# Kernel optimization log

Hardware: AMD Instinct MI355X
Metric: run time of the kernel (lower is better)

The kernel has to match this reference:

```python
import jax, jax.numpy as jnp
import numpy as np

B, L, DIN, DOUT, H, N, NLAYERS, NRES, NSPECIES = 32, 2048, 5, 5, 256, 32, 4, 3, 100


def conv1d(x, w, b, pad):
    # x: (B, Cin, L), w: (Cout, Cin, K)
    y = jax.lax.conv_general_dilated(x, w, (1,), [(pad, pad)], dimension_numbers=('NCH', 'OIH', 'NCH'))
    return y + b[None, :, None]


def layer_norm_c(x, g, b):
    # LayerNorm over channel dim of (B, H, L) (matches norm(x.transpose(-1,-2)).transpose(-1,-2))
    mu = x.mean(1, keepdims=True)
    v = ((x - mu) ** 2).mean(1, keepdims=True)
    return (x - mu) / jnp.sqrt(v + 1e-5) * g[None, :, None] + b[None, :, None]


def dss_layer(x, log_dt, lam_re, lam_im, W_re, W_im, D, glu_w, glu_b):
    # Bidirectional diagonal state-space (DSS) layer, transposed layout (B, H, L).
    Bb, Hh, Ll = x.shape
    dt = jnp.exp(log_dt)                                  # (H,)
    lam = lam_re + 1j * lam_im                            # (N,) with Re(lam) < 0
    pos = jnp.arange(Ll)
    # Vandermonde: E[h,n,l] = exp(dt[h] * lam[n] * l)
    E = jnp.exp(dt[:, None, None] * lam[None, :, None] * pos[None, None, :])  # (H,N,L) complex
    W = W_re + 1j * W_im                                  # (2,H,N) fwd/bwd kernels
    k = jnp.einsum('chn,hnl->chl', W, E).real             # (2,H,L)
    zpad = jnp.zeros_like(k[0])
    k2 = jnp.concatenate([k[0], zpad], -1) + jnp.concatenate([zpad, k[1][:, ::-1]], -1)  # (H,2L)
    # FFT circular conv of length 2L -> linear conv, keep first L
    y = jnp.fft.irfft(jnp.fft.rfft(x, 2 * Ll) * jnp.fft.rfft(k2, 2 * Ll)[None], 2 * Ll)[..., :Ll]
    y = y + D[None, :, None] * x
    y = jax.nn.gelu(y, approximate=False)
    # postact GLU via position-wise linear H -> 2H
    z = jnp.einsum('oh,bhl->bol', glu_w, y) + glu_b[None, :, None]
    return z[:, :Hh] * jax.nn.sigmoid(z[:, Hh:])


def setup_inputs():
    key = jax.random.key(0)
    ks = jax.random.split(key, 20)
    g = lambda i, shape, s=0.05: jax.random.normal(ks[i], shape, jnp.float32) * s
    inp = {}
    inp['x'] = jax.random.normal(ks[0], (B, DIN, L), jnp.float32)
    inp['xs'] = jax.random.randint(ks[1], (B,), 0, NSPECIES)
    inp['enc_w'] = g(2, (H, DIN, 15))
    inp['enc_b'] = jnp.zeros((H,), jnp.float32)
    inp['res_w1'] = g(3, (NRES, H, H, 3), 0.02)
    inp['res_b1'] = jnp.zeros((NRES, H), jnp.float32)
    inp['res_w2'] = g(4, (NRES, H, H, 3), 0.02)
    inp['res_b2'] = jnp.zeros((NRES, H), jnp.float32)
    inp['log_dt'] = jax.random.uniform(ks[5], (NLAYERS, H), jnp.float32, float(np.log(1e-3)), float(np.log(1e-1)))
    inp['lam_re'] = -(0.1 + jax.random.uniform(ks[6], (NLAYERS, N), jnp.float32))
    inp['lam_im'] = jnp.broadcast_to(jnp.pi * jnp.arange(N, dtype=jnp.float32), (NLAYERS, N)) + 0.0
    inp['W_re'] = g(7, (NLAYERS, 2, H, N), 0.1)
    inp['W_im'] = g(8, (NLAYERS, 2, H, N), 0.1)
    inp['D'] = g(9, (NLAYERS, H), 1.0)
    inp['glu_w'] = g(10, (NLAYERS, 2 * H, H))
    inp['glu_b'] = jnp.zeros((NLAYERS, 2 * H), jnp.float32)
    inp['ln_g'] = jnp.ones((NLAYERS, H), jnp.float32)
    inp['ln_b'] = jnp.zeros((NLAYERS, H), jnp.float32)
    inp['dec_w'] = g(11, (DOUT, H, 15))
    inp['dec_b'] = jnp.zeros((DOUT,), jnp.float32)
    inp['sp_emb'] = g(12, (NSPECIES, H), 0.02)
    inp['h1_w'] = g(13, (128, 256)); inp['h1_b'] = jnp.zeros((128,), jnp.float32)
    inp['h2_w'] = g(14, (64, 128)); inp['h2_b'] = jnp.zeros((64,), jnp.float32)
    inp['h3_w'] = g(15, (32, 64)); inp['h3_b'] = jnp.zeros((32,), jnp.float32)
    inp['h4_w'] = g(16, (1, 32)); inp['h4_b'] = jnp.zeros((1,), jnp.float32)
    return inp


def _forward(x, xs, enc_w, enc_b, res_w1, res_b1, res_w2, res_b2, log_dt, lam_re, lam_im, W_re, W_im, D, glu_w, glu_b, ln_g, ln_b, dec_w, dec_b, sp_emb, h1_w, h1_b, h2_w, h2_b, h3_w, h3_b, h4_w, h4_b):
    h = conv1d(x, enc_w, enc_b, 7)
    for i in range(NRES):  # L1Block resnet stack (dropout/BN are identity at eval)
        r = jax.nn.relu(conv1d(h, res_w1[i], res_b1[i], 1))
        r = conv1d(r, res_w2[i], res_b2[i], 1)
        h = jax.nn.relu(r + h)
    for i in range(NLAYERS):  # post-norm DSS blocks
        z = dss_layer(h, log_dt[i], lam_re[i], lam_im[i], W_re[i], W_im[i], D[i], glu_w[i], glu_b[i])
        h = layer_norm_c(z + h, ln_g[i], ln_b[i])
    h = h + sp_emb[xs][:, :, None]  # species encoder (embed_before=False)
    seq_emb = h
    agg = h.mean(-1)  # (B, H)
    r = jax.nn.elu(agg @ h1_w.T + h1_b)
    r = jax.nn.elu(r @ h2_w.T + h2_b)
    r = jax.nn.elu(r @ h3_w.T + h3_b)
    reg_y = r @ h4_w.T + h4_b
    dec = conv1d(h, dec_w, dec_b, 7)
    return dec, seq_emb, reg_y


def reference(x, xs, enc_w, enc_b, res_w1, res_b1, res_w2, res_b2, log_dt, lam_re, lam_im, W_re, W_im, D, glu_w, glu_b, ln_g, ln_b, dec_w, dec_b, sp_emb, h1_w, h1_b, h2_w, h2_b, h3_w, h3_b, h4_w, h4_b):
    return _forward(x, xs, enc_w, enc_b, res_w1, res_b1, res_w2, res_b2, log_dt, lam_re, lam_im, W_re, W_im, D, glu_w, glu_b, ln_g, ln_b, dec_w, dec_b, sp_emb, h1_w, h1_b, h2_w, h2_b, h3_w, h3_b, h4_w, h4_b)
```

## Files before the change

kernel.cpp:

```cpp
#include <hip/hip_runtime.h>
#include <math.h>

#define B 32
#define L 2048
#define DIN 5
#define DOUT 5
#define H 256
#define NST 32
#define NLAYERS 4
#define NRES 3
#define CHUNK 128
#define NCH 16
#define LSEQ (B*H*L)

typedef __attribute__((ext_vector_type(8))) _Float16 half8;
typedef __attribute__((ext_vector_type(4))) float f32x4;

__device__ __forceinline__ float gelu_exact(float v) {
    return 0.5f * v * (1.0f + erff(v * 0.7071067811865475f));
}
#define SWZ(r) ((((r) ^ ((r) >> 2)) & 3))
#define LDIDX(l, c) ((l)*281 + ((c)>>5)*35 + ((c)&31))

__global__ void k_wenc(const float* __restrict__ ew, _Float16* __restrict__ wenc) {
    int idx = blockIdx.x*256 + threadIdx.x;
    if (idx >= 256*96) return;
    int o = idx / 96, kk = idx % 96;
    int ci = kk >> 4, k = kk & 15;
    float v = (ci < DIN && k < 15) ? ew[(o*DIN + ci)*15 + k] : 0.f;
    wenc[idx] = (_Float16)v;
}

__global__ __launch_bounds__(256) void k_enc(const float* __restrict__ x,
        const _Float16* __restrict__ wenc, const float* __restrict__ bias,
        _Float16* __restrict__ out) {
    __shared__ _Float16 a_lds[3*128*32];
    __shared__ _Float16 b_lds[3*128*32];
    const int tid = threadIdx.x;
    const int mbase = blockIdx.x * 128;
    const int oh = blockIdx.y;
    const int b = mbase >> 11;
    const int lbase = mbase & 2047;
    const int lane = tid & 63;
    const int w = tid >> 6;
    const int wm = (w >> 1) * 64, wn = (w & 1) * 64;
    const int fr = lane & 15, kg = lane >> 4;

    #pragma unroll
    for (int i = 0; i < 6; ++i) {
        int g = i*256 + tid;
        int r = g / 12, rem = g % 12;
        int ks = rem >> 2, q = rem & 3;
        int kk0 = ks*32 + q*8;
        int ci = kk0 >> 4, k0 = kk0 & 15;
        half8 va;
        #pragma unroll
        for (int e = 0; e < 8; ++e) {
            int k = k0 + e;
            int l = lbase + r - 7 + k;
            float v = (ci < DIN && k < 15 && l >= 0 && l < L)
                        ? x[((size_t)(b*DIN + ci))*L + l] : 0.f;
            va[e] = (_Float16)v;
        }
        *(half8*)&a_lds[ks*4096 + r*32 + ((q ^ SWZ(r))*8)] = va;
        uint4 vb = *(const uint4*)&wenc[(size_t)(oh*128 + r)*96 + kk0];
        *(uint4*)&b_lds[ks*4096 + r*32 + ((q ^ SWZ(r))*8)] = vb;
    }
    __syncthreads();
    f32x4 acc[4][4];
    #pragma unroll
    for (int i = 0; i < 4; ++i)
        #pragma unroll
        for (int j = 0; j < 4; ++j)
            #pragma unroll
            for (int k = 0; k < 4; ++k) acc[i][j][k] = 0.f;
    #pragma unroll
    for (int ks = 0; ks < 3; ++ks) {
        half8 af[4], bfr[4];
        #pragma unroll
        for (int mf = 0; mf < 4; ++mf) {
            int ra = wm + mf*16 + fr;
            af[mf] = *(const half8*)&a_lds[ks*4096 + ra*32 + ((kg ^ SWZ(ra))*8)];
        }
        #pragma unroll
        for (int nf = 0; nf < 4; ++nf) {
            int rb = wn + nf*16 + fr;
            bfr[nf] = *(const half8*)&b_lds[ks*4096 + rb*32 + ((kg ^ SWZ(rb))*8)];
        }
        #pragma unroll
        for (int mf = 0; mf < 4; ++mf)
            #pragma unroll
            for (int nf = 0; nf < 4; ++nf)
                acc[mf][nf] = __builtin_amdgcn_mfma_f32_16x16x32_f16(af[mf], bfr[nf], acc[mf][nf], 0, 0, 0);
    }
    #pragma unroll
    for (int nf = 0; nf < 4; ++nf) {
        int o = oh*128 + wn + nf*16 + fr;
        float bo = bias[o];
        #pragma unroll
        for (int mf = 0; mf < 4; ++mf)
            #pragma unroll
            for (int rg = 0; rg < 4; ++rg) {
                size_t m = (size_t)mbase + wm + mf*16 + kg*4 + rg;
                out[m*256 + o] = (_Float16)(acc[mf][nf][rg] + bo);
            }
// ... 180 lines not shown
__global__ __launch_bounds__(128) void k_wzp(const float4* __restrict__ zw,
        _Float16* __restrict__ zp) {
    int hh = blockIdx.x;
    int t = threadIdx.x;
    int dn = t >> 1, c = t & 1, dir = dn >> 5, n = dn & 31;
    float4 z4 = zw[hh*NST + n];
    float zre = z4.x, zim = z4.y;
    _Float16* dst = &zp[(size_t)hh*16384 + t*128];
    float cr = 1.f, ci = 0.f;
    for (int p = 0; p < 128; ++p) {
        float val = c ? ci : cr;
        dst[dir ? p : (127 - p)] = (_Float16)val;
        float nr = cr*zre - ci*zim;
        float ni = cr*zim + ci*zre;
        cr = nr; ci = ni;
    }
}

__global__ __launch_bounds__(128) void k_wkern(const float* __restrict__ log_dt,
        const float* __restrict__ lam_re, const float* __restrict__ lam_im,
        const float* __restrict__ W_re, const float* __restrict__ W_im,
        _Float16* __restrict__ wbig, int layer) {
    __shared__ float kf[128], kb[128];
    __shared__ float E[128*129];
    const int hh = blockIdx.x;
    const int t = threadIdx.x;
    float dt = expf(log_dt[layer*H + hh]);
    float skf = 0.f, skb = 0.f;
    for (int n = 0; n < 32; ++n) {
        float a  = dt * lam_re[layer*NST + n];
        float bi = dt * lam_im[layer*NST + n];
        float wfr = W_re[((layer*2+0)*H + hh)*NST + n];
        float wfi = W_im[((layer*2+0)*H + hh)*NST + n];
        float wbr = W_re[((layer*2+1)*H + hh)*NST + n];
        float wbi = W_im[((layer*2+1)*H + hh)*NST + n];
        float e0 = expf(a*t), s0, c0; sincosf(bi*t, &s0, &c0);
        float zr0 = e0*c0, zi0 = e0*s0;
        skf = fmaf(wfr, zr0, skf) - wfi*zi0;
        skb = fmaf(wbr, zr0, skb) - wbi*zi0;
        float e1 = expf(a*(t+1)), s1, c1; sincosf(bi*(t+1), &s1, &c1);
        float zr1 = e1*c1, zi1 = e1*s1;
        E[t*129 + n]      = wfr*zr1 - wfi*zi1;
        E[t*129 + 32 + n] = -(wfr*zi1 + wfi*zr1);
        float e2 = expf(a*(127-t)), s2, c2; sincosf(bi*(127-t), &s2, &c2);
        float zr2 = e2*c2, zi2 = e2*s2;
        E[t*129 + 64 + n] = wbr*zr2 - wbi*zi2;
        E[t*129 + 96 + n] = -(wbr*zi2 + wbi*zr2);
    }
    kf[t] = skf; kb[t] = skb;
    __syncthreads();
    _Float16* dst = &wbig[(size_t)hh*32768];
    for (int idx = t; idx < 128*256; idx += 128) {
        int tt = idx >> 8, k = idx & 255;
        float v;
        if (k < 128) v = (k <= tt) ? kf[tt - k] : kb[k - tt - 1];
        else         v = E[tt*129 + (k - 128)];
        dst[idx] = (_Float16)v;
    }
}

__global__ void k_wtg16(const float* __restrict__ gw, _Float16* __restrict__ wg, int layer) {
    int idx = blockIdx.x*256 + threadIdx.x;
    if (idx >= 512*256) return;
    wg[idx] = (_Float16)gw[layer*512*256 + idx];
}

__global__ void k_wdec(const float* __restrict__ dw, _Float16* __restrict__ wdk) {
    int idx = blockIdx.x*256 + threadIdx.x;
    if (idx >= 15*16*256) return;
    int cfull = idx & 255;
    int o = (idx >> 8) & 15;
    int k = idx >> 12;
    float v = (o < DOUT) ? dw[(o*H + cfull)*15 + k] : 0.f;
    int cc = cfull >> 5, cl = cfull & 31;
    int cq = cl >> 3, cb = cl & 7;
    wdk[cc*7680 + (k*16 + o)*32 + ((cq ^ SWZ(o))*8) + cb] = (_Float16)v;
}

__global__ __launch_bounds__(256) void k_dss(const _Float16* __restrict__ hm16,
        const _Float16* __restrict__ zp, const _Float16* __restrict__ wbig,
        const float4* __restrict__ zwb, const float* __restrict__ Dv,
        _Float16* __restrict__ y16, int layer) {
    __shared__ _Float16 xbuf[4*64*32];
    __shared__ _Float16 bbuf[2*128*32];
    __shared__ float    sbuf[64*128];
    _Float16* sb16 = (_Float16*)sbuf;

    const int tid = threadIdx.x;
    const int hh = blockIdx.x;
    const int b0 = blockIdx.y * 4;
    const int lane = tid & 63;
    const int w = tid >> 6;
    const int wn = w * 32;
    const int fr = lane & 15, kg = lane >> 4;

    #pragma unroll
    for (int i = 0; i < 4; ++i) {
        int g = i*256 + tid;
        int m = g >> 4, gi = g & 15;
        int kc = gi >> 2, q = gi & 3;
        uint4 v = *(const uint4*)&hm16[((size_t)((b0 + (m>>4))*H + hh))*L
                                       + (m&15)*128 + kc*32 + q*8];
        *(uint4*)&xbuf[kc*2048 + m*32 + ((q ^ SWZ(m))*8)] = v;
    }

    f32x4 acc1[4][2];
    #pragma unroll
    for (int i = 0; i < 4; ++i)
        #pragma unroll
        for (int j = 0; j < 2; ++j)
            #pragma unroll
            for (int k = 0; k < 4; ++k) acc1[i][j][k] = 0.f;
    const _Float16* zb = &zp[(size_t)hh*16384];
    const int gr0 = tid >> 2, gq0 = tid & 3;
    const int gr1 = 64 + gr0;
    uint4 pb0 = *(const uint4*)&zb[gr0*128 + gq0*8];
    uint4 pb1 = *(const uint4*)&zb[gr1*128 + gq0*8];
    for (int kc = 0; kc < 4; ++kc) {
        __syncthreads();
        *(uint4*)&bbuf[(kc&1)*4096 + gr0*32 + ((gq0 ^ SWZ(gr0))*8)] = pb0;
        *(uint4*)&bbuf[(kc&1)*4096 + gr1*32 + ((gq0 ^ SWZ(gr1))*8)] = pb1;
        if (kc < 3) {
            pb0 = *(const uint4*)&zb[gr0*128 + (kc+1)*32 + gq0*8];
            pb1 = *(const uint4*)&zb[gr1*128 + (kc+1)*32 + gq0*8];
        }
        __syncthreads();
        half8 af[4], bf2[2];
        #pragma unroll
        for (int mf = 0; mf < 4; ++mf) {
            int ra = mf*16 + fr;
            af[mf] = *(const half8*)&xbuf[kc*2048 + ra*32 + ((kg ^ SWZ(ra))*8)];
        }
        #pragma unroll
        for (int nf = 0; nf < 2; ++nf) {
            int rb = wn + nf*16 + fr;
            bf2[nf] = *(const half8*)&bbuf[(kc&1)*4096 + rb*32 + ((kg ^ SWZ(rb))*8)];
        }
        #pragma unroll
        for (int mf = 0; mf < 4; ++mf)
            #pragma unroll
            for (int nf = 0; nf < 2; ++nf)
                acc1[mf][nf] = __builtin_amdgcn_mfma_f32_16x16x32_f16(af[mf], bf2[nf], acc1[mf][nf], 0, 0, 0);
    }
    #pragma unroll
    for (int mf = 0; mf < 4; ++mf)
        #pragma unroll
        for (int nf = 0; nf < 2; ++nf)
            #pragma unroll
            for (int rg = 0; rg < 4; ++rg)
                sbuf[(mf*16 + kg*4 + rg)*128 + wn + nf*16 + fr] = acc1[mf][nf][rg];
    __syncthreads();

    {
        int b_loc = tid >> 6, dn = tid & 63;
        int dir = dn >> 5, n = dn & 31;
        float4 z4 = zwb[hh*NST + n];
        float zcre = z4.z, zcim = z4.w;
        int q1 = n >> 3, e1 = n & 7;
        float pre = 0.f, pim = 0.f;
        for (int s = 0; s < NCH; ++s) {
            int ch = dir ? (NCH - 1 - s) : s;
            int m = b_loc*16 + ch;
            bbuf[(dir*2 + 0)*2048 + m*32 + ((q1 ^ SWZ(m))*8) + e1] = (_Float16)pre;
            bbuf[(dir*2 + 1)*2048 + m*32 + ((q1 ^ SWZ(m))*8) + e1] = (_Float16)pim;
            float cre = sbuf[m*128 + dn*2];
            float cim = sbuf[m*128 + dn*2 + 1];
            float nre = fmaf(zcre, pre, fmaf(-zcim, pim, cre));
            float nim = fmaf(zcre, pim, fmaf(zcim, pre, cim));
            pre = nre; pim = nim;
        }
    }
    __syncthreads();

    f32x4 acc3[4][2];
    #pragma unroll
    for (int i = 0; i < 4; ++i)
        #pragma unroll
        for (int j = 0; j < 2; ++j)
            #pragma unroll
            for (int k = 0; k < 4; ++k) acc3[i][j][k] = 0.f;
    const _Float16* wb = &wbig[(size_t)hh*32768];
    pb0 = *(const uint4*)&wb[gr0*256 + gq0*8];
    pb1 = *(const uint4*)&wb[gr1*256 + gq0*8];
    for (int kc = 0; kc < 8; ++kc) {
        __syncthreads();
        *(uint4*)&sb16[(kc&1)*4096 + gr0*32 + ((gq0 ^ SWZ(gr0))*8)] = pb0;
        *(uint4*)&sb16[(kc&1)*4096 + gr1*32 + ((gq0 ^ SWZ(gr1))*8)] = pb1;
        if (kc < 7) {
            pb0 = *(const uint4*)&wb[gr0*256 + (kc+1)*32 + gq0*8];
            pb1 = *(const uint4*)&wb[gr1*256 + (kc+1)*32 + gq0*8];
        }
        __syncthreads();
        half8 af[4], bf2[2];
        #pragma unroll
        for (int mf = 0; mf < 4; ++mf) {
            int ra = mf*16 + fr;
            af[mf] = (kc < 4)
                ? *(const half8*)&xbuf[kc*2048 + ra*32 + ((kg ^ SWZ(ra))*8)]
                : *(const half8*)&bbuf[(kc-4)*2048 + ra*32 + ((kg ^ SWZ(ra))*8)];
        }
        #pragma unroll
        for (int nf = 0; nf < 2; ++nf) {
            int rb = wn + nf*16 + fr;
            bf2[nf] = *(const half8*)&sb16[(kc&1)*4096 + rb*32 + ((kg ^ SWZ(rb))*8)];
        }
        #pragma unroll
        for (int mf = 0; mf < 4; ++mf)
            #pragma unroll
            for (int nf = 0; nf < 2; ++nf)
                acc3[mf][nf] = __builtin_amdgcn_mfma_f32_16x16x32_f16(af[mf], bf2[nf], acc3[mf][nf], 0, 0, 0);
    }
    __syncthreads();
    float dv = Dv[layer*H + hh];
    _Float16* yst = bbuf;
    #pragma unroll
    for (int mf = 0; mf < 4; ++mf) {
        #pragma unroll
        for (int rg = 0; rg < 4; ++rg) {
            int m = mf*16 + kg*4 + rg;
            #pragma unroll
            for (int nf = 0; nf < 2; ++nf) {
                int t = wn + nf*16 + fr;
                float xv = (float)xbuf[(t>>5)*2048 + m*32 + ((((t&31)>>3) ^ SWZ(m))*8) + (t&7)];
                float v = acc3[mf][nf][rg] + dv * xv;
                yst[m*128 + t] = (_Float16)gelu_exact(v);
            }
        }
    }
    __syncthreads();
    {
        int r = tid >> 2, tc = (tid & 3) * 32;
        size_t gb = ((size_t)((b0 + (r>>4))*H + hh))*L + (r&15)*128;
        #pragma unroll
        for (int u = 0; u < 4; ++u)
            *(half8*)&y16[gb + tc + u*8] = *(half8*)&yst[r*128 + tc + u*8];
    }
}

__global__ __launch_bounds__(256) void k_glu16(const _Float16* __restrict__ yt,
        const _Float16* __restrict__ wg, const float* __restrict__ bias,
        _Float16* __restrict__ zc) {
    __shared__ _Float16 a_lds[128*32];
    __shared__ _Float16 b_lds[128*32];
    __shared__ float    ep[32*64];
    const int tid = threadIdx.x;
    const int mbase = blockIdx.x * 128;
    const int o0 = blockIdx.y * 64;
    const int lane = tid & 63;
    const int w = tid >> 6;
    const int wm = (w >> 1) * 64, wn = (w & 1) * 32;
    const int fr = lane & 15, kg = lane >> 4;
    const int r0s = tid >> 2, q0 = tid & 3;
    const int r1s = 64 + r0s;
    const int aw0 = r0s*32 + ((q0 ^ SWZ(r0s)) * 8);
    const int aw1 = r1s*32 + ((q0 ^ SWZ(r1s)) * 8);
    const int og0 = o0 + r0s;
    const int og1 = 256 + o0 + r0s;

    f32x4 accg[4][2], accs[4][2];
    #pragma unroll
    for (int i = 0; i < 4; ++i)
        #pragma unroll
        for (int j = 0; j < 2; ++j)
            #pragma unroll
            for (int k = 0; k < 4; ++k) { accg[i][j][k] = 0.f; accs[i][j][k] = 0.f; }

    uint4 pa0, pa1, pb0, pb1;
    auto loadstep = [&](int kc, uint4& a0, uint4& a1, uint4& b0, uint4& b1) {
        const int cb = kc*32 + q0*8;
        a0 = *(const uint4*)&yt[((size_t)(mbase + r0s))*256 + cb];
        a1 = *(const uint4*)&yt[((size_t)(mbase + r1s))*256 + cb];
        b0 = *(const uint4*)&wg[((size_t)og0)*256 + cb];
        b1 = *(const uint4*)&wg[((size_t)og1)*256 + cb];
    };
    loadstep(0, pa0, pa1, pb0, pb1);
    for (int kc = 0; kc < 8; ++kc) {
        __syncthreads();
        *(uint4*)&a_lds[aw0] = pa0;
        *(uint4*)&a_lds[aw1] = pa1;
        *(uint4*)&b_lds[aw0] = pb0;
        *(uint4*)&b_lds[aw1] = pb1;
        uint4 na0 = make_uint4(0,0,0,0), na1 = na0, nb0 = na0, nb1 = na0;
        if (kc < 7) loadstep(kc+1, na0, na1, nb0, nb1);
        __syncthreads();
        half8 af[4], bg[2], bs[2];
        #pragma unroll
        for (int mf = 0; mf < 4; ++mf) {
            int ra = wm + mf*16 + fr;
            af[mf] = *(const half8*)&a_lds[ra*32 + ((kg ^ SWZ(ra)) * 8)];
        }
        #pragma unroll
        for (int nf = 0; nf < 2; ++nf) {
            int rb = wn + nf*16 + fr;
            bg[nf] = *(const half8*)&b_lds[rb*32 + ((kg ^ SWZ(rb)) * 8)];
            int rb2 = 64 + rb;
            bs[nf] = *(const half8*)&b_lds[rb2*32 + ((kg ^ SWZ(rb2)) * 8)];
        }
        #pragma unroll
        for (int mf = 0; mf < 4; ++mf)
            #pragma unroll
            for (int nf = 0; nf < 2; ++nf) {
                accg[mf][nf] = __builtin_amdgcn_mfma_f32_16x16x32_f16(af[mf], bg[nf], accg[mf][nf], 0, 0, 0);
                accs[mf][nf] = __builtin_amdgcn_mfma_f32_16x16x32_f16(af[mf], bs[nf], accs[mf][nf], 0, 0, 0);
            }
        pa0 = na0; pa1 = na1; pb0 = nb0; pb1 = nb1;
    }
    float b0v[2], b1v[2];
    #pragma unroll
    for (int nf = 0; nf < 2; ++nf) {
        int o = o0 + wn + nf*16 + fr;
        b0v[nf] = bias[o]; b1v[nf] = bias[256 + o];
    }
    const int er = tid >> 3, eoc = (tid & 7) * 8;
    #pragma unroll
    for (int mf = 0; mf < 4; ++mf) {
        __syncthreads();
        #pragma unroll
        for (int nf = 0; nf < 2; ++nf) {
            int ol = wn + nf*16 + fr;
            int srb = (w >> 1)*16 + kg*4;
            #pragma unroll
            for (int rg = 0; rg < 4; ++rg) {
                float g = accg[mf][nf][rg] + b0v[nf];
                float s = accs[mf][nf][rg] + b1v[nf];
                ep[(srb + rg)*64 + ol] = g / (1.f + expf(-s));
            }
        }
        __syncthreads();
        size_t m = (size_t)mbase + mf*16 + (er < 16 ? er : 48 + er);
        float4 v0 = *(float4*)&ep[er*64 + eoc];
        float4 v1 = *(float4*)&ep[er*64 + eoc + 4];
        half8 hv;
        hv[0]=(_Float16)v0.x; hv[1]=(_Float16)v0.y; hv[2]=(_Float16)v0.z; hv[3]=(_Float16)v0.w;
        hv[4]=(_Float16)v1.x; hv[5]=(_Float16)v1.y; hv[6]=(_Float16)v1.z; hv[7]=(_Float16)v1.w;
        *(half8*)&zc[m*256 + o0 + eoc] = hv;
    }
}

template<bool SP>
__global__ __launch_bounds__(256) void k_ln2(const _Float16* __restrict__ zc,
        _Float16* __restrict__ hm, const float* __restrict__ g, const float* __restrict__ bb,
        const int* __restrict__ xs, const float* __restrict__ emb,
        float* __restrict__ outseq) {
    __shared__ float tl[8992];
    int tid = threadIdx.x;
    int b = blockIdx.y;
    int l0 = blockIdx.x * 32;
    for (int j = tid; j < 1024; j += 256) {
        int c = j >> 2, l8 = (j & 3) * 8;
        half8 v = *(const half8*)&hm[((size_t)(b*H + c))*L + l0 + l8];
        #pragma unroll
        for (int e = 0; e < 8; ++e) tl[LDIDX(l8 + e, c)] = (float)v[e];
    }
    __syncthreads();
    int r = tid >> 3, p = tid & 7;
    float v[32];
    float sum = 0.f, ss = 0.f;
    const _Float16* zrow = &zc[((size_t)(b*L + l0 + r))*256 + p*32];
    #pragma unroll
    for (int q = 0; q < 4; ++q) {
        half8 z8 = *(const half8*)&zrow[q*8];
        #pragma unroll
        for (int i = 0; i < 8; ++i) {
            float hv = tl[LDIDX(r, p*32 + q*8 + i)];
            float vv = (float)z8[i] + hv;
            v[q*8+i] = vv;
            sum += vv; ss = fmaf(vv, vv, ss);
        }
    }
    sum += __shfl_xor(sum, 1); ss += __shfl_xor(ss, 1);
    sum += __shfl_xor(sum, 2); ss += __shfl_xor(ss, 2);
    sum += __shfl_xor(sum, 4); ss += __shfl_xor(ss, 4);
    float mu = sum * (1.f/256.f);
    float var = ss * (1.f/256.f) - mu*mu;
    float rs = rsqrtf(var + 1e-5f);
    int sp = SP ? xs[b] : 0;
    #pragma unroll
    for (int q = 0; q < 32; ++q) {
        int c = p*32 + q;
        float val = (v[q] - mu) * rs * g[c] + bb[c];
        if (SP) val += emb[sp*H + c];
        tl[LDIDX(r, c)] = val;
    }
    __syncthreads();
    for (int j = tid; j < 1024; j += 256) {
        int c = j >> 2, l8 = (j & 3) * 8;
        float fv[8];
        half8 hv;
        #pragma unroll
        for (int e = 0; e < 8; ++e) {
            fv[e] = tl[LDIDX(l8 + e, c)];
            hv[e] = (_Float16)fv[e];
        }
        *(half8*)&hm[((size_t)(b*H + c))*L + l0 + l8] = hv;
        if (SP) {
            *(float4*)&outseq[((size_t)(b*H + c))*L + l0 + l8] = make_float4(fv[0],fv[1],fv[2],fv[3]);
            *(float4*)&outseq[((size_t)(b*H + c))*L + l0 + l8 + 4] = make_float4(fv[4],fv[5],fv[6],fv[7]);
        }
    }
}

__global__ __launch_bounds__(128) void k_dec(const _Float16* __restrict__ ht,
        const _Float16* __restrict__ wdk, const float* __restrict__ bias,
        float* __restrict__ outdec) {
    __shared__ _Float16 a_lds[160*32];
    __shared__ _Float16 b_lds[15*16*32];
    const int tid = threadIdx.x;
    const int mbase = blockIdx.x * 128;
    const int b = mbase >> 11;
    const int lbase = mbase & 2047;
    const int lane = tid & 63;
    const int w = tid >> 6;
    const int fr = lane & 15, kg = lane >> 4;
    const int rs = tid >> 2, q0 = tid & 3;
    f32x4 acc[4];
    #pragma unroll
    for (int i = 0; i < 4; ++i)
        #pragma unroll
        for (int k = 0; k < 4; ++k) acc[i][k] = 0.f;
    for (int cc = 0; cc < 8; ++cc) {
        __syncthreads();
        #pragma unroll
        for (int ps = 0; ps < 5; ++ps) {
            int r = ps*32 + rs;
            if (r < 142) {
                int l = lbase - 7 + r;
                uint4 v = (l >= 0 && l < L) ? *(const uint4*)&ht[((size_t)(b*L + l))*256 + cc*32 + q0*8]
                                            : make_uint4(0,0,0,0);
                *(uint4*)&a_lds[r*32 + ((q0 ^ SWZ(r))*8)] = v;
            }
        }
        for (int jj = tid; jj < 960; jj += 128)
            *(uint4*)&b_lds[jj*8] = *(const uint4*)&wdk[cc*7680 + jj*8];
        __syncthreads();
        #pragma unroll
        for (int k = 0; k < 15; ++k) {
            half8 bfr = *(const half8*)&b_lds[(k*16 + fr)*32 + ((kg ^ SWZ(fr))*8)];
            #pragma unroll
            for (int mf = 0; mf < 4; ++mf) {
                int ra = w*64 + mf*16 + fr + k;
                half8 af = *(const half8*)&a_lds[ra*32 + ((kg ^ SWZ(ra))*8)];
                acc[mf] = __builtin_amdgcn_mfma_f32_16x16x32_f16(af, bfr, acc[mf], 0, 0, 0);
            }
        }
    }
    if (fr < DOUT) {
        float bo = bias[fr];
        #pragma unroll
        for (int mf = 0; mf < 4; ++mf)
            #pragma unroll
            for (int rg = 0; rg < 4; ++rg) {
                int m = mbase + w*64 + mf*16 + kg*4 + rg;
                outdec[((size_t)(b*DOUT + fr))*L + (m & 2047)] = acc[mf][rg] + bo;
            }
    }
}

__global__ __launch_bounds__(256) void k_agg(const _Float16* __restrict__ h, float* __restrict__ agg) {
    __shared__ float red[256];
    int bc = blockIdx.x;
    int tid = threadIdx.x;
    half8 v = *(const half8*)&h[(size_t)bc*L + tid*8];
    float s = 0.f;
    #pragma unroll
    for (int e = 0; e < 8; ++e) s += (float)v[e];
    red[tid] = s; __syncthreads();
    for (int k = 128; k > 0; k >>= 1) {
        if (tid < k) red[tid] += red[tid+k];
        __syncthreads();
    }
    if (tid == 0) agg[bc] = red[0] * (1.f/(float)L);
}

__global__ __launch_bounds__(128) void k_mlp(const float* __restrict__ agg,
        const float* __restrict__ w1, const float* __restrict__ b1,
        const float* __restrict__ w2, const float* __restrict__ b2,
        const float* __restrict__ w3, const float* __restrict__ b3,
        const float* __restrict__ w4, const float* __restrict__ b4,
        float* __restrict__ outreg) {
    __shared__ float a0[256], r1[128], r2[64], r3[32];
    int b = blockIdx.x, tid = threadIdx.x;
    a0[tid] = agg[b*256 + tid];
    a0[tid+128] = agg[b*256 + tid + 128];
    __syncthreads();
    {
        float s = b1[tid];
        for (int k = 0; k < 256; ++k) s = fmaf(w1[tid*256+k], a0[k], s);
        r1[tid] = s > 0.f ? s : expm1f(s);
    }
    __syncthreads();
    if (tid < 64) {
        float s = b2[tid];
        for (int k = 0; k < 128; ++k) s = fmaf(w2[tid*128+k], r1[k], s);
        r2[tid] = s > 0.f ? s : expm1f(s);
    }
    __syncthreads();
    if (tid < 32) {
        float s = b3[tid];
        for (int k = 0; k < 64; ++k) s = fmaf(w3[tid*64+k], r2[k], s);
        r3[tid] = s > 0.f ? s : expm1f(s);
    }
    __syncthreads();
    if (tid == 0) {
        float s = b4[0];
        for (int k = 0; k < 32; ++k) s = fmaf(w4[k], r3[k], s);
        outreg[b] = s;
    }
}

extern "C" void kernel_launch(void* const* d_in, const int* in_sizes, int n_in,
                              void* d_out, int out_size, void* d_ws, size_t ws_size,
                              hipStream_t stream) {
    const float* x      = (const float*)d_in[0];
    const int*   xs     = (const int*)d_in[1];
    const float* enc_w  = (const float*)d_in[2];
    const float* enc_b  = (const float*)d_in[3];
    const float* res_w1 = (const float*)d_in[4];
    const float* res_b1 = (const float*)d_in[5];
    const float* res_w2 = (const float*)d_in[6];
    const float* res_b2 = (const float*)d_in[7];
    const float* log_dt = (const float*)d_in[8];
    const float* lam_re = (const float*)d_in[9];
    const float* lam_im = (const float*)d_in[10];
    const float* W_re   = (const float*)d_in[11];
    const float* W_im   = (const float*)d_in[12];
    const float* Dv     = (const float*)d_in[13];
    const float* glu_w  = (const float*)d_in[14];
    const float* glu_b  = (const float*)d_in[15];
    const float* ln_g   = (const float*)d_in[16];
    const float* ln_b   = (const float*)d_in[17];
    const float* dec_w  = (const float*)d_in[18];
    const float* dec_b  = (const float*)d_in[19];
    const float* sp_emb = (const float*)d_in[20];
    const float* h1_w = (const float*)d_in[21]; const float* h1_b = (const float*)d_in[22];
    const float* h2_w = (const float*)d_in[23]; const float* h2_b = (const float*)d_in[24];
    const float* h3_w = (const float*)d_in[25]; const float* h3_b = (const float*)d_in[26];
    const float* h4_w = (const float*)d_in[27]; const float* h4_b = (const float*)d_in[28];

    float* ws   = (float*)d_ws;
    _Float16* hm16 = (_Float16*)ws;
    float* t1   = ws + (size_t)LSEQ;
    float* t2   = ws + (size_t)2*LSEQ;
    _Float16* xb  = (_Float16*)t1;
    _Float16* xa  = (_Float16*)t1 + (size_t)LSEQ;
    _Float16* wpk = (_Float16*)t2;
    _Float16* yt   = (_Float16*)t1;
    _Float16* wbig = (_Float16*)t1 + (size_t)LSEQ;
    _Float16* zp   = wbig + (size_t)H*32768;
    _Float16* y16  = (_Float16*)t2;
    _Float16* zc16 = (_Float16*)t2;
    _Float16* dect = (_Float16*)t1;
    float* tail = ws + (size_t)3*LSEQ;
    _Float16* wg  = (_Float16*)tail;
    float4* zwb = (float4*)(tail + 65536);
    float* aggb = tail + 65536 + 32768;
    _Float16* wdk = (_Float16*)(aggb + 8192);
    _Float16* wenc = wdk + 61440;

    float* outdec = (float*)d_out;
    float* outseq = outdec + B*DOUT*L;
    float* outreg = outseq + (size_t)LSEQ;

    k_wenc<<<96, 256, 0, stream>>>(enc_w, wenc);
    k_enc<<<dim3(B*L/128, 2), 256, 0, stream>>>(x, wenc, enc_b, xa);

    k_wpack<<<(NRES*2*3*65536 + 255)/256, 256, 0, stream>>>(res_w1, res_w2, wpk);
    for (int r = 0; r < NRES; ++r) {
        k_cv3<false><<<B*L/128, 256, 0, stream>>>(
            xa, wpk + (size_t)(r*2+0)*3*65536, res_b1 + r*H, nullptr, xb);
        k_cv3<true><<<B*L/128, 256, 0, stream>>>(
            xb, wpk + (size_t)(r*2+1)*3*65536, res_b2 + r*H, xa, xa);
    }
    k_t_cf16<<<dim3(L/64, H/64, B), 256, 0, stream>>>(xa, hm16);

    for (int i = 0; i < NLAYERS; ++i) {
        k_zw<<<(H*NST + 255)/256, 256, 0, stream>>>(log_dt, lam_re, lam_im, zwb, i);
        k_wzp<<<H, 128, 0, stream>>>(zwb, zp);
        k_wkern<<<H, 128, 0, stream>>>(log_dt, lam_re, lam_im, W_re, W_im, wbig, i);
        k_wtg16<<<(512*256 + 255)/256, 256, 0, stream>>>(glu_w, wg, i);
        k_dss<<<dim3(H, 8), 256, 0, stream>>>(hm16, zp, wbig, zwb, Dv, y16, i);
        k_t16<<<dim3(L/64, H/64, B), 256, 0, stream>>>(y16, yt);
        k_glu16<<<dim3(B*L/128, 4), 256, 0, stream>>>(yt, wg, glu_b + i*512, zc16);
        if (i < NLAYERS - 1)
            k_ln2<false><<<dim3(L/32, B), 256, 0, stream>>>(zc16, hm16, ln_g + i*H, ln_b + i*H,
                                                            nullptr, nullptr, nullptr);
        else
            k_ln2<true><<<dim3(L/32, B), 256, 0, stream>>>(zc16, hm16, ln_g + i*H, ln_b + i*H,
                                                           xs, sp_emb, outseq);
    }

    k_agg<<<B*H, 256, 0, stream>>>(hm16, aggb);
    k_mlp<<<B, 128, 0, stream>>>(aggb, h1_w, h1_b, h2_w, h2_b, h3_w, h3_b, h4_w, h4_b, outreg);
    k_t16<<<dim3(L/64, H/64, B), 256, 0, stream>>>(hm16, dect);
    k_wdec<<<(15*16*256 + 255)/256, 256, 0, stream>>>(dec_w, wdk);
    k_dec<<<B*L/128, 128, 0, stream>>>(dect, wdk, dec_b, outdec);
}
```

Baseline: 1.147 ms.

## Fuse transpose, GLU GEMM and LayerNorm into one kernel; preload DSS kernel weights

Replaces the separate transpose, GLU GEMM and residual LayerNorm kernels with one fused kernel. It reads the channel-major DSS output directly, computes both GLU halves for all 256 channels over a 64-position tile, adds the residual and applies LayerNorm in registers and shared memory. This removes two intermediate fp16 round trips through global memory and two launches per layer. In k_dss the Z-projection weights are loaded into LDS all at once, and the second GEMM stages 64-wide K chunks, which halves the barrier count. The cost is more registers (accg/accs 4x4) and large LDS in the fused kernel, which may limit occupancy.

```diff
diff --git a/kernel.cpp b/kernel.cpp
--- a/kernel.cpp
+++ b/kernel.cpp
@@ -20,7 +20,6 @@
     return 0.5f * v * (1.0f + erff(v * 0.7071067811865475f));
 }
 #define SWZ(r) ((((r) ^ ((r) >> 2)) & 3))
-#define LDIDX(l, c) ((l)*281 + ((c)>>5)*35 + ((c)&31))
 
 __global__ void k_wenc(const float* __restrict__ ew, _Float16* __restrict__ wenc) {
     int idx = blockIdx.x*256 + threadIdx.x;
@@ -367,9 +366,8 @@
         const float4* __restrict__ zwb, const float* __restrict__ Dv,
         _Float16* __restrict__ y16, int layer) {
     __shared__ _Float16 xbuf[4*64*32];
-    __shared__ _Float16 bbuf[2*128*32];
-    __shared__ float    sbuf[64*128];
-    _Float16* sb16 = (_Float16*)sbuf;
+    __shared__ _Float16 zsb[16384];
+    __shared__ _Float16 bbuf[4*64*32];
 
     const int tid = threadIdx.x;
     const int hh = blockIdx.x;
@@ -388,6 +386,16 @@
                                        + (m&15)*128 + kc*32 + q*8];
         *(uint4*)&xbuf[kc*2048 + m*32 + ((q ^ SWZ(m))*8)] = v;
     }
+    const _Float16* zb = &zp[(size_t)hh*16384];
+    #pragma unroll
+    for (int i = 0; i < 8; ++i) {
+        int g = i*256 + tid;
+        int kc = g >> 9, rem = g & 511;
+        int t = rem >> 2, q = rem & 3;
+        uint4 v = *(const uint4*)&zb[t*128 + kc*32 + q*8];
+        *(uint4*)&zsb[kc*4096 + t*32 + ((q ^ SWZ(t))*8)] = v;
+    }
+    __syncthreads();
 
     f32x4 acc1[4][2];
     #pragma unroll
@@ -396,20 +404,8 @@
         for (int j = 0; j < 2; ++j)
             #pragma unroll
             for (int k = 0; k < 4; ++k) acc1[i][j][k] = 0.f;
-    const _Float16* zb = &zp[(size_t)hh*16384];
-    const int gr0 = tid >> 2, gq0 = tid & 3;
-    const int gr1 = 64 + gr0;
-    uint4 pb0 = *(const uint4*)&zb[gr0*128 + gq0*8];
-    uint4 pb1 = *(const uint4*)&zb[gr1*128 + gq0*8];
+    #pragma unroll
     for (int kc = 0; kc < 4; ++kc) {
-        __syncthreads();
-        *(uint4*)&bbuf[(kc&1)*4096 + gr0*32 + ((gq0 ^ SWZ(gr0))*8)] = pb0;
-        *(uint4*)&bbuf[(kc&1)*4096 + gr1*32 + ((gq0 ^ SWZ(gr1))*8)] = pb1;
-        if (kc < 3) {
-            pb0 = *(const uint4*)&zb[gr0*128 + (kc+1)*32 + gq0*8];
-            pb1 = *(const uint4*)&zb[gr1*128 + (kc+1)*32 + gq0*8];
-        }
-        __syncthreads();
         half8 af[4], bf2[2];
         #pragma unroll
         for (int mf = 0; mf < 4; ++mf) {
@@ -419,7 +415,7 @@
         #pragma unroll
         for (int nf = 0; nf < 2; ++nf) {
             int rb = wn + nf*16 + fr;
-            bf2[nf] = *(const half8*)&bbuf[(kc&1)*4096 + rb*32 + ((kg ^ SWZ(rb))*8)];
+            bf2[nf] = *(const half8*)&zsb[kc*4096 + rb*32 + ((kg ^ SWZ(rb))*8)];
         }
         #pragma unroll
         for (int mf = 0; mf < 4; ++mf)
@@ -427,13 +423,15 @@
             for (int nf = 0; nf < 2; ++nf)
                 acc1[mf][nf] = __builtin_amdgcn_mfma_f32_16x16x32_f16(af[mf], bf2[nf], acc1[mf][nf], 0, 0, 0);
     }
+    __syncthreads();
+    float* sfp = (float*)zsb;
     #pragma unroll
     for (int mf = 0; mf < 4; ++mf)
         #pragma unroll
         for (int nf = 0; nf < 2; ++nf)
             #pragma unroll
             for (int rg = 0; rg < 4; ++rg)
-                sbuf[(mf*16 + kg*4 + rg)*128 + wn + nf*16 + fr] = acc1[mf][nf][rg];
+                sfp[(mf*16 + kg*4 + rg)*128 + wn + nf*16 + fr] = acc1[mf][nf][rg];
     __syncthreads();
 
     {
@@ -448,8 +446,8 @@
             int m = b_loc*16 + ch;
             bbuf[(dir*2 + 0)*2048 + m*32 + ((q1 ^ SWZ(m))*8) + e1] = (_Float16)pre;
             bbuf[(dir*2 + 1)*2048 + m*32 + ((q1 ^ SWZ(m))*8) + e1] = (_Float16)pim;
-            float cre = sbuf[m*128 + dn*2];
-            float cim = sbuf[m*128 + dn*2 + 1];
+            float cre = sfp[m*128 + dn*2];
+            float cim = sfp[m*128 + dn*2 + 1];
             float nre = fmaf(zcre, pre, fmaf(-zcim, pim, cre));
             float nim = fmaf(zcre, pim, fmaf(zcim, pre, cim));
             pre = nre; pim = nim;
@@ -465,35 +463,50 @@
             #pragma unroll
             for (int k = 0; k < 4; ++k) acc3[i][j][k] = 0.f;
     const _Float16* wb = &wbig[(size_t)hh*32768];
-    pb0 = *(const uint4*)&wb[gr0*256 + gq0*8];
-    pb1 = *(const uint4*)&wb[gr1*256 + gq0*8];
-    for (int kc = 0; kc < 8; ++kc) {
-        __syncthreads();
-        *(uint4*)&sb16[(kc&1)*4096 + gr0*32 + ((gq0 ^ SWZ(gr0))*8)] = pb0;
-        *(uint4*)&sb16[(kc&1)*4096 + gr1*32 + ((gq0 ^ SWZ(gr1))*8)] = pb1;
-        if (kc < 7) {
-            pb0 = *(const uint4*)&wb[gr0*256 + (kc+1)*32 + gq0*8];
-            pb1 = *(const uint4*)&wb[gr1*256 + (kc+1)*32 + gq0*8];
-        }
-        __syncthreads();
-        half8 af[4], bf2[2];
-        #pragma unroll
-        for (int mf = 0; mf < 4; ++mf) {
-            int ra = mf*16 + fr;
-            af[mf] = (kc < 4)
-                ? *(const half8*)&xbuf[kc*2048 + ra*32 + ((kg ^ SWZ(ra))*8)]
-                : *(const half8*)&bbuf[(kc-4)*2048 + ra*32 + ((kg ^ SWZ(ra))*8)];
-        }
-        #pragma unroll
-        for (int nf = 0; nf < 2; ++nf) {
-            int rb = wn + nf*16 + fr;
-            bf2[nf] = *(const half8*)&sb16[(kc&1)*4096 + rb*32 + ((kg ^ SWZ(rb))*8)];
-        }
-        #pragma unroll
-        for (int mf = 0; mf < 4; ++mf)
-            #pragma unroll
-            for (int nf = 0; nf < 2; ++nf)
-                acc3[mf][nf] = __builtin_amdgcn_mfma_f32_16x16x32_f16(af[mf], bf2[nf], acc3[mf][nf], 0, 0, 0);
+    uint4 wr[4];
+    auto loadW = [&](int p, uint4 (&r)[4]) {
+        #pragma unroll
+        for (int i = 0; i < 4; ++i) {
+            int g = i*256 + tid;
+            int sub = g >> 9, rem = g & 511;
+            int t = rem >> 2, q = rem & 3;
+            r[i] = *(const uint4*)&wb[t*256 + p*64 + sub*32 + q*8];
+        }
+    };
+    loadW(0, wr);
+    for (int p = 0; p < 4; ++p) {
+        __syncthreads();
+        #pragma unroll
+        for (int i = 0; i < 4; ++i) {
+            int g = i*256 + tid;
+            int sub = g >> 9, rem = g & 511;
+            int t = rem >> 2, q = rem & 3;
+            *(uint4*)&zsb[(p&1)*8192 + sub*4096 + t*32 + ((q ^ SWZ(t))*8)] = wr[i];
+        }
+        if (p < 3) loadW(p+1, wr);
+        __syncthreads();
+        #pragma unroll
+        for (int sub = 0; sub < 2; ++sub) {
+            int kcg = p*2 + sub;
+            half8 af[4], bf2[2];
+            #pragma unroll
+            for (int mf = 0; mf < 4; ++mf) {
+                int ra = mf*16 + fr;
+                af[mf] = (kcg < 4)
+                    ? *(const half8*)&xbuf[kcg*2048 + ra*32 + ((kg ^ SWZ(ra))*8)]
+                    : *(const half8*)&bbuf[(kcg-4)*2048 + ra*32 + ((kg ^ SWZ(ra))*8)];
+            }
+            #pragma unroll
+            for (int nf = 0; nf < 2; ++nf) {
+                int rb = wn + nf*16 + fr;
+                bf2[nf] = *(const half8*)&zsb[(p&1)*8192 + sub*4096 + rb*32 + ((kg ^ SWZ(rb))*8)];
+            }
+            #pragma unroll
+            for (int mf = 0; mf < 4; ++mf)
+                #pragma unroll
+                for (int nf = 0; nf < 2; ++nf)
+                    acc3[mf][nf] = __builtin_amdgcn_mfma_f32_16x16x32_f16(af[mf], bf2[nf], acc3[mf][nf], 0, 0, 0);
+        }
     }
     __syncthreads();
     float dv = Dv[layer*H + hh];
@@ -522,165 +535,177 @@
     }
 }
 
-__global__ __launch_bounds__(256) void k_glu16(const _Float16* __restrict__ yt,
+template<bool SP>
+__global__ __launch_bounds__(256, 2) void k_gluln(const _Float16* __restrict__ y16,
         const _Float16* __restrict__ wg, const float* __restrict__ bias,
-        _Float16* __restrict__ zc) {
-    __shared__ _Float16 a_lds[128*32];
-    __shared__ _Float16 b_lds[128*32];
-    __shared__ float    ep[32*64];
-    const int tid = threadIdx.x;
-    const int mbase = blockIdx.x * 128;
-    const int o0 = blockIdx.y * 64;
-    const int lane = tid & 63;
-    const int w = tid >> 6;
-    const int wm = (w >> 1) * 64, wn = (w & 1) * 32;
-    const int fr = lane & 15, kg = lane >> 4;
-    const int r0s = tid >> 2, q0 = tid & 3;
-    const int r1s = 64 + r0s;
-    const int aw0 = r0s*32 + ((q0 ^ SWZ(r0s)) * 8);
-    const int aw1 = r1s*32 + ((q0 ^ SWZ(r1s)) * 8);
-    const int og0 = o0 + r0s;
-    const int og1 = 256 + o0 + r0s;
-
-    f32x4 accg[4][2], accs[4][2];
-    #pragma unroll
-    for (int i = 0; i < 4; ++i)
-        #pragma unroll
-        for (int j = 0; j < 2; ++j)
-            #pragma unroll
-            for (int k = 0; k < 4; ++k) { accg[i][j][k] = 0.f; accs[i][j][k] = 0.f; }
-
-    uint4 pa0, pa1, pb0, pb1;
-    auto loadstep = [&](int kc, uint4& a0, uint4& a1, uint4& b0, uint4& b1) {
-        const int cb = kc*32 + q0*8;
-        a0 = *(const uint4*)&yt[((size_t)(mbase + r0s))*256 + cb];
-        a1 = *(const uint4*)&yt[((size_t)(mbase + r1s))*256 + cb];
-        b0 = *(const uint4*)&wg[((size_t)og0)*256 + cb];
-        b1 = *(const uint4*)&wg[((size_t)og1)*256 + cb];
-    };
-    loadstep(0, pa0, pa1, pb0, pb1);
-    for (int kc = 0; kc < 8; ++kc) {
-        __syncthreads();
-        *(uint4*)&a_lds[aw0] = pa0;
-        *(uint4*)&a_lds[aw1] = pa1;
-        *(uint4*)&b_lds[aw0] = pb0;
-        *(uint4*)&b_lds[aw1] = pb1;
-        uint4 na0 = make_uint4(0,0,0,0), na1 = na0, nb0 = na0, nb1 = na0;
-        if (kc < 7) loadstep(kc+1, na0, na1, nb0, nb1);
-        __syncthreads();
-        half8 af[4], bg[2], bs[2];
-        #pragma unroll
-        for (int mf = 0; mf < 4; ++mf) {
-            int ra = wm + mf*16 + fr;
-            af[mf] = *(const half8*)&a_lds[ra*32 + ((kg ^ SWZ(ra)) * 8)];
-        }
-        #pragma unroll
-        for (int nf = 0; nf < 2; ++nf) {
-            int rb = wn + nf*16 + fr;
-            bg[nf] = *(const half8*)&b_lds[rb*32 + ((kg ^ SWZ(rb)) * 8)];
-            int rb2 = 64 + rb;
-            bs[nf] = *(const half8*)&b_lds[rb2*32 + ((kg ^ SWZ(rb2)) * 8)];
-        }
-        #pragma unroll
-        for (int mf = 0; mf < 4; ++mf)
-            #pragma unroll
-            for (int nf = 0; nf < 2; ++nf) {
-                accg[mf][nf] = __builtin_amdgcn_mfma_f32_16x16x32_f16(af[mf], bg[nf], accg[mf][nf], 0, 0, 0);
-                accs[mf][nf] = __builtin_amdgcn_mfma_f32_16x16x32_f16(af[mf], bs[nf], accs[mf][nf], 0, 0, 0);
-            }
-        pa0 = na0; pa1 = na1; pb0 = nb0; pb1 = nb1;
-    }
-    float b0v[2], b1v[2];
-    #pragma unroll
-    for (int nf = 0; nf < 2; ++nf) {
-        int o = o0 + wn + nf*16 + fr;
-        b0v[nf] = bias[o]; b1v[nf] = bias[256 + o];
-    }
-    const int er = tid >> 3, eoc = (tid & 7) * 8;
-    #pragma unroll
-    for (int mf = 0; mf < 4; ++mf) {
-        __syncthreads();
-        #pragma unroll
-        for (int nf = 0; nf < 2; ++nf) {
-            int ol = wn + nf*16 + fr;
-            int srb = (w >> 1)*16 + kg*4;
-            #pragma unroll
-            for (int rg = 0; rg < 4; ++rg) {
-                float g = accg[mf][nf][rg] + b0v[nf];
-                float s = accs[mf][nf][rg] + b1v[nf];
-                ep[(srb + rg)*64 + ol] = g / (1.f + expf(-s));
-            }
-        }
-        __syncthreads();
-        size_t m = (size_t)mbase + mf*16 + (er < 16 ? er : 48 + er);
-        float4 v0 = *(float4*)&ep[er*64 + eoc];
-        float4 v1 = *(float4*)&ep[er*64 + eoc + 4];
-        half8 hv;
-        hv[0]=(_Float16)v0.x; hv[1]=(_Float16)v0.y; hv[2]=(_Float16)v0.z; hv[3]=(_Float16)v0.w;
-        hv[4]=(_Float16)v1.x; hv[5]=(_Float16)v1.y; hv[6]=(_Float16)v1.z; hv[7]=(_Float16)v1.w;
-        *(half8*)&zc[m*256 + o0 + eoc] = hv;
-    }
-}
-
-template<bool SP>
-__global__ __launch_bounds__(256) void k_ln2(const _Float16* __restrict__ zc,
         _Float16* __restrict__ hm, const float* __restrict__ g, const float* __restrict__ bb,
         const int* __restrict__ xs, const float* __restrict__ emb,
         float* __restrict__ outseq) {
-    __shared__ float tl[8992];
-    int tid = threadIdx.x;
-    int b = blockIdx.y;
-    int l0 = blockIdx.x * 32;
-    for (int j = tid; j < 1024; j += 256) {
-        int c = j >> 2, l8 = (j & 3) * 8;
-        half8 v = *(const half8*)&hm[((size_t)(b*H + c))*L + l0 + l8];
-        #pragma unroll
-        for (int e = 0; e < 8; ++e) tl[LDIDX(l8 + e, c)] = (float)v[e];
-    }
-    __syncthreads();
-    int r = tid >> 3, p = tid & 7;
-    float v[32];
-    float sum = 0.f, ss = 0.f;
-    const _Float16* zrow = &zc[((size_t)(b*L + l0 + r))*256 + p*32];
-    #pragma unroll
-    for (int q = 0; q < 4; ++q) {
-        half8 z8 = *(const half8*)&zrow[q*8];
+    __shared__ _Float16 a_lds[64*32];
+    __shared__ _Float16 b_lds[512*32];
+    __shared__ _Float16 hmbuf[256*72];
+    __shared__ float psum[256], pss[256], mur[64], rsr[64];
+
+    const int tid = threadIdx.x;
+    const int mbase = blockIdx.x * 64;
+    const int b = mbase >> 11;
+    const int l0 = mbase & 2047;
+    const int lane = tid & 63;
+    const int w = tid >> 6;
+    const int fr = lane & 15, kg = lane >> 4;
+    const int ac = tid >> 3, al8 = (tid & 7) * 8;
+
+    f32x4 accg[4][4], accs[4][4];
+    #pragma unroll
+    for (int i = 0; i < 4; ++i)
+        #pragma unroll
+        for (int j = 0; j < 4; ++j)
+            #pragma unroll
+            for (int k = 0; k < 4; ++k) { accg[i][j][k] = 0.f; accs[i][j][k] = 0.f; }
+
+    uint4 aR, bR[8];
+    auto loadA = [&](int kc) -> uint4 {
+        return *(const uint4*)&y16[((size_t)(b*256 + kc*32 + ac))*2048 + l0 + al8];
+    };
+    auto loadB = [&](int kc, uint4 (&r)[8]) {
         #pragma unroll
         for (int i = 0; i < 8; ++i) {
-            float hv = tl[LDIDX(r, p*32 + q*8 + i)];
-            float vv = (float)z8[i] + hv;
-            v[q*8+i] = vv;
-            sum += vv; ss = fmaf(vv, vv, ss);
-        }
-    }
-    sum += __shfl_xor(sum, 1); ss += __shfl_xor(ss, 1);
-    sum += __shfl_xor(sum, 2); ss += __shfl_xor(ss, 2);
-    sum += __shfl_xor(sum, 4); ss += __shfl_xor(ss, 4);
-    float mu = sum * (1.f/256.f);
-    float var = ss * (1.f/256.f) - mu*mu;
-    float rs = rsqrtf(var + 1e-5f);
+            int gq = i*256 + tid;
+            int row = gq >> 2, q = gq & 3;
+            r[i] = *(const uint4*)&wg[(size_t)row*256 + kc*32 + q*8];
+        }
+    };
+    aR = loadA(0); loadB(0, bR);
+    for (int kc = 0; kc < 8; ++kc) {
+        __syncthreads();
+        {
+            union { uint4 u; half8 h; } av; av.u = aR;
+            int q = ac >> 3, e0 = ac & 7;
+            #pragma unroll
+            for (int e = 0; e < 8; ++e) {
+                int l = al8 + e;
+                a_lds[l*32 + ((q ^ SWZ(l))*8) + e0] = av.h[e];
+            }
+        }
+        #pragma unroll
+        for (int i = 0; i < 8; ++i) {
+            int gq = i*256 + tid;
+            int row = gq >> 2, q = gq & 3;
+            *(uint4*)&b_lds[row*32 + ((q ^ SWZ(row))*8)] = bR[i];
+        }
+        if (kc < 7) { aR = loadA(kc+1); loadB(kc+1, bR); }
+        __syncthreads();
+        half8 af[4];
+        #pragma unroll
+        for (int mf = 0; mf < 4; ++mf) {
+            int ra = mf*16 + fr;
+            af[mf] = *(const half8*)&a_lds[ra*32 + ((kg ^ SWZ(ra))*8)];
+        }
+        #pragma unroll
+        for (int nf = 0; nf < 4; ++nf) {
+            int rg_ = w*64 + nf*16 + fr;
+            half8 bg = *(const half8*)&b_lds[rg_*32 + ((kg ^ SWZ(rg_))*8)];
+            int rs_ = 256 + rg_;
+            half8 bs = *(const half8*)&b_lds[rs_*32 + ((kg ^ SWZ(rs_))*8)];
+            #pragma unroll
+            for (int mf = 0; mf < 4; ++mf) {
+                accg[mf][nf] = __builtin_amdgcn_mfma_f32_16x16x32_f16(af[mf], bg, accg[mf][nf], 0, 0, 0);
+                accs[mf][nf] = __builtin_amdgcn_mfma_f32_16x16x32_f16(af[mf], bs, accs[mf][nf], 0, 0, 0);
+            }
+        }
+    }
+    __syncthreads();
+    #pragma unroll
+    for (int i = 0; i < 8; ++i) {
+        int gq = i*256 + tid;
+        int c = gq >> 3, m8 = (gq & 7) * 8;
+        half8 v = *(const half8*)&hm[((size_t)(b*256 + c))*2048 + l0 + m8];
+        *(half8*)&hmbuf[c*72 + m8] = v;
+    }
+    int cl_[4];
+    float b0v[4], b1v[4], gv[4], bbv[4], ev[4];
     int sp = SP ? xs[b] : 0;
     #pragma unroll
-    for (int q = 0; q < 32; ++q) {
-        int c = p*32 + q;
-        float val = (v[q] - mu) * rs * g[c] + bb[c];
-        if (SP) val += emb[sp*H + c];
-        tl[LDIDX(r, c)] = val;
-    }
-    __syncthreads();
-    for (int j = tid; j < 1024; j += 256) {
-        int c = j >> 2, l8 = (j & 3) * 8;
-        float fv[8];
-        half8 hv;
-        #pragma unroll
-        for (int e = 0; e < 8; ++e) {
-            fv[e] = tl[LDIDX(l8 + e, c)];
-            hv[e] = (_Float16)fv[e];
-        }
-        *(half8*)&hm[((size_t)(b*H + c))*L + l0 + l8] = hv;
+    for (int nf = 0; nf < 4; ++nf) {
+        int c = w*64 + nf*16 + fr;
+        cl_[nf] = c;
+        b0v[nf] = bias[c]; b1v[nf] = bias[256 + c];
+        gv[nf] = g[c]; bbv[nf] = bb[c];
+        ev[nf] = SP ? emb[sp*H + c] : 0.f;
+    }
+    __syncthreads();
+    float sum_m[16], ss_m[16];
+    #pragma unroll
+    for (int mf = 0; mf < 4; ++mf) {
+        #pragma unroll
+        for (int rg = 0; rg < 4; ++rg) {
+            int m = mf*16 + kg*4 + rg;
+            float s = 0.f, q2 = 0.f;
+            #pragma unroll
+            for (int nf = 0; nf < 4; ++nf) {
+                float gg = accg[mf][nf][rg] + b0v[nf];
+                float sg = accs[mf][nf][rg] + b1v[nf];
+                float z = gg / (1.f + expf(-sg));
+                float v = z + (float)hmbuf[cl_[nf]*72 + m];
+                accg[mf][nf][rg] = v;
+                s += v; q2 = fmaf(v, v, q2);
+            }
+            sum_m[mf*4 + rg] = s; ss_m[mf*4 + rg] = q2;
+        }
+    }
+    #pragma unroll
+    for (int d = 1; d < 16; d <<= 1) {
+        #pragma unroll
+        for (int mi = 0; mi < 16; ++mi) {
+            sum_m[mi] += __shfl_xor(sum_m[mi], d);
+            ss_m[mi]  += __shfl_xor(ss_m[mi], d);
+        }
+    }
+    if (fr == 0) {
+        #pragma unroll
+        for (int mf = 0; mf < 4; ++mf)
+            #pragma unroll
+            for (int rg = 0; rg < 4; ++rg) {
+                int m = mf*16 + kg*4 + rg;
+                psum[m*4 + w] = sum_m[mf*4 + rg];
+                pss[m*4 + w]  = ss_m[mf*4 + rg];
+            }
+    }
+    __syncthreads();
+    if (tid < 64) {
+        float s = psum[tid*4] + psum[tid*4+1] + psum[tid*4+2] + psum[tid*4+3];
+        float q2 = pss[tid*4] + pss[tid*4+1] + pss[tid*4+2] + pss[tid*4+3];
+        float mu = s * (1.f/256.f);
+        float var = q2 * (1.f/256.f) - mu*mu;
+        mur[tid] = mu;
+        rsr[tid] = rsqrtf(var + 1e-5f);
+    }
+    __syncthreads();
+    #pragma unroll
+    for (int mf = 0; mf < 4; ++mf) {
+        #pragma unroll
+        for (int rg = 0; rg < 4; ++rg) {
+            int m = mf*16 + kg*4 + rg;
+            float mu = mur[m], rs = rsr[m];
+            #pragma unroll
+            for (int nf = 0; nf < 4; ++nf) {
+                float val = (accg[mf][nf][rg] - mu) * rs * gv[nf] + bbv[nf] + ev[nf];
+                hmbuf[cl_[nf]*72 + m] = (_Float16)val;
+            }
+        }
+    }
+    __syncthreads();
+    #pragma unroll
+    for (int i = 0; i < 8; ++i) {
+        int gq = i*256 + tid;
+        int c = gq >> 3, m8 = (gq & 7) * 8;
+        half8 hv = *(const half8*)&hmbuf[c*72 + m8];
+        *(half8*)&hm[((size_t)(b*256 + c))*2048 + l0 + m8] = hv;
         if (SP) {
-            *(float4*)&outseq[((size_t)(b*H + c))*L + l0 + l8] = make_float4(fv[0],fv[1],fv[2],fv[3]);
-            *(float4*)&outseq[((size_t)(b*H + c))*L + l0 + l8 + 4] = make_float4(fv[4],fv[5],fv[6],fv[7]);
+            float4 f0 = make_float4((float)hv[0], (float)hv[1], (float)hv[2], (float)hv[3]);
+            float4 f1 = make_float4((float)hv[4], (float)hv[5], (float)hv[6], (float)hv[7]);
+            *(float4*)&outseq[((size_t)(b*256 + c))*2048 + l0 + m8] = f0;
+            *(float4*)&outseq[((size_t)(b*256 + c))*2048 + l0 + m8 + 4] = f1;
         }
     }
 }
@@ -829,11 +854,9 @@
     _Float16* xb  = (_Float16*)t1;
     _Float16* xa  = (_Float16*)t1 + (size_t)LSEQ;
     _Float16* wpk = (_Float16*)t2;
-    _Float16* yt   = (_Float16*)t1;
     _Float16* wbig = (_Float16*)t1 + (size_t)LSEQ;
     _Float16* zp   = wbig + (size_t)H*32768;
     _Float16* y16  = (_Float16*)t2;
-    _Float16* zc16 = (_Float16*)t2;
     _Float16* dect = (_Float16*)t1;
     float* tail = ws + (size_t)3*LSEQ;
     _Float16* wg  = (_Float16*)tail;
@@ -864,14 +887,12 @@
         k_wkern<<<H, 128, 0, stream>>>(log_dt, lam_re, lam_im, W_re, W_im, wbig, i);
         k_wtg16<<<(512*256 + 255)/256, 256, 0, stream>>>(glu_w, wg, i);
         k_dss<<<dim3(H, 8), 256, 0, stream>>>(hm16, zp, wbig, zwb, Dv, y16, i);
-        k_t16<<<dim3(L/64, H/64, B), 256, 0, stream>>>(y16, yt);
-        k_glu16<<<dim3(B*L/128, 4), 256, 0, stream>>>(yt, wg, glu_b + i*512, zc16);
         if (i < NLAYERS - 1)
-            k_ln2<false><<<dim3(L/32, B), 256, 0, stream>>>(zc16, hm16, ln_g + i*H, ln_b + i*H,
-                                                            nullptr, nullptr, nullptr);
+            k_gluln<false><<<B*L/64, 256, 0, stream>>>(y16, wg, glu_b + i*512, hm16,
+                    ln_g + i*H, ln_b + i*H, nullptr, nullptr, nullptr);
         else
-            k_ln2<true><<<dim3(L/32, B), 256, 0, stream>>>(zc16, hm16, ln_g + i*H, ln_b + i*H,
-                                                           xs, sp_emb, outseq);
+            k_gluln<true><<<B*L/64, 256, 0, stream>>>(y16, wg, glu_b + i*512, hm16,
+                    ln_g + i*H, ln_b + i*H, xs, sp_emb, outseq);
     }
 
     k_agg<<<B*H, 256, 0, stream>>>(hm16, aggb);
```

New measurement: 1.246 ms. 8.6% more time.
